# Performance work log

Measured on AMD Instinct MI355X. Metric: run time of the kernel, lower is better.

## Reference

```python
import jax, jax.numpy as jnp
import numpy as np

DIM = 128
HID = 128


def setup_inputs() -> dict:
    key = jax.random.key(0)
    ks = jax.random.split(key, 7)
    x = jax.random.normal(ks[0], (1, 256, 512, DIM), dtype=jnp.float32)
    s = 1.0 / np.sqrt(DIM)
    return {
        "x": x,
        "ln_g": jnp.ones((DIM,), jnp.float32),
        "ln_b": jnp.zeros((DIM,), jnp.float32),
        "w_left": jax.random.normal(ks[1], (DIM, HID), jnp.float32) * s,
        "b_left": jnp.zeros((HID,), jnp.float32),
        "w_right": jax.random.normal(ks[2], (DIM, HID), jnp.float32) * s,
        "b_right": jnp.zeros((HID,), jnp.float32),
        "w_out": jax.random.normal(ks[3], (HID, DIM), jnp.float32) * (1.0 / np.sqrt(HID)),
        "b_out": jnp.zeros((DIM,), jnp.float32),
    }


def reference(x, ln_g, ln_b, w_left, b_left, w_right, b_right, w_out, b_out):
    # LayerNorm over last dim (eps matches torch default 1e-5)
    mu = jnp.mean(x, axis=-1, keepdims=True)
    var = jnp.mean(jnp.square(x - mu), axis=-1, keepdims=True)
    xn = (x - mu) * jax.lax.rsqrt(var + 1e-5) * ln_g + ln_b
    # dual projections: (b, m, i, h)
    left = jnp.einsum('bmid,dh->bmih', xn, w_left) + b_left
    right = jnp.einsum('bmjd,dh->bmjh', xn, w_right) + b_right
    # mean over m of (left_i + right_j) == mean_m(left)_i + mean_m(right)_j
    # (exact algebraic identity; avoids the (b,m,i,j,h) intermediate)
    left_m = jnp.mean(left, axis=1)   # (b, i, h)
    right_m = jnp.mean(right, axis=1)  # (b, j, h)
    outer = left_m[:, :, None, :] + right_m[:, None, :, :]  # (b, i, j, h)
    return jnp.einsum('bijh,hd->bijd', outer, w_out) + b_out
```

## Files before the change

### kernel.cpp

```cpp
#include <hip/hip_runtime.h>
#include <hip/hip_bf16.h>


#define DIM 128
#define NI  512
#define NM  256

__global__ __launch_bounds__(512) void ln_mean_kernel(
    const float* __restrict__ x,
    const float* __restrict__ ln_g,
    const float* __restrict__ ln_b,
    float* __restrict__ S)
{
    const int i    = blockIdx.x;
    const int tid  = threadIdx.x;
    const int lane = tid & 63;
    const int wave = tid >> 6;

    const float g0  = ln_g[2*lane];
    const float g1  = ln_g[2*lane + 1];
    const float be0 = ln_b[2*lane];
    const float be1 = ln_b[2*lane + 1];

    float acc0 = 0.f, acc1 = 0.f;

    #pragma unroll 4
    for (int t = 0; t < NM/8; ++t) {
        const int m = wave + (t << 3);
        const float2 v = *(const float2*)(x + (((size_t)(m * NI + i)) << 7) + 2*lane);

        float s  = v.x + v.y;
        float s2 = v.x*v.x + v.y*v.y;
        #pragma unroll
        for (int off = 32; off; off >>= 1) {
            s  += __shfl_xor(s,  off);
            s2 += __shfl_xor(s2, off);
        }
        const float mu   = s * (1.f/128.f);
        const float var  = s2 * (1.f/128.f) - mu*mu;
        const float rstd = rsqrtf(var + 1e-5f);

        acc0 += (v.x - mu) * rstd * g0 + be0;
        acc1 += (v.y - mu) * rstd * g1 + be1;
    }

    __shared__ float red0[512];
    __shared__ float red1[512];
    red0[tid] = acc0;
    red1[tid] = acc1;
    __syncthreads();

    if (tid < 64) {
        float a0 = 0.f, a1 = 0.f;
        #pragma unroll
        for (int w = 0; w < 8; ++w) {
            a0 += red0[(w << 6) + tid];
            a1 += red1[(w << 6) + tid];
        }
        float2 r;
        r.x = a0 * (1.f/(float)NM);
        r.y = a1 * (1.f/(float)NM);
        *(float2*)(S + ((size_t)i << 7) + 2*tid) = r;
    }
}

__global__ __launch_bounds__(256) void project_kernel(
    const float* __restrict__ S,
    const float* __restrict__ w_left,  const float* __restrict__ b_left,
    const float* __restrict__ w_right, const float* __restrict__ b_right,
    const float* __restrict__ w_out,   const float* __restrict__ b_out,
    float* __restrict__ L, float* __restrict__ R)
{
    const int i   = blockIdx.x;
    const int tid = threadIdx.x;
    const int h   = tid & 127;
    const bool isR = (tid >= 128);

    __shared__ float sS[128];
    __shared__ float sTL[128];
    __shared__ float sTR[128];

    if (tid < 128) sS[tid] = S[((size_t)i << 7) + tid];
    __syncthreads();

    const float* W = isR ? w_right : w_left;
    float acc = isR ? b_right[h] : b_left[h];
    #pragma unroll 8
    for (int d = 0; d < DIM; ++d) {
        acc += sS[d] * W[(d << 7) + h];
    }
    (isR ? sTR : sTL)[h] = acc;
    __syncthreads();

    const float* T = isR ? sTR : sTL;
    float acc2 = isR ? b_out[h] : 0.f;
    #pragma unroll 8
    for (int hh = 0; hh < DIM; ++hh) {
        acc2 += T[hh] * w_out[(hh << 7) + h];
    }
    (isR ? R : L)[((size_t)i << 7) + h] = acc2;
}

__global__ __launch_bounds__(256) void expand_kernel(
    const float4* __restrict__ L4,
    const float4* __restrict__ R4,
    float4* __restrict__ out4)
{
    const size_t t = (size_t)blockIdx.x * 256 + threadIdx.x;
    const int d4 = (int)(t & 31);
    const int j  = (int)((t >> 5) & 511);
    const int i  = (int)(t >> 14);

    const float4 a = L4[(i << 5) + d4];
    const float4 b = R4[(j << 5) + d4];
    float4 o;
    o.x = a.x + b.x;
    o.y = a.y + b.y;
    o.z = a.z + b.z;
    o.w = a.w + b.w;
    out4[t] = o;
}

extern "C" void kernel_launch(void* const* d_in, const int* in_sizes, int n_in,
                              void* d_out, int out_size, void* d_ws, size_t ws_size,
                              hipStream_t stream) {
    const float* x       = (const float*)d_in[0];
    const float* ln_g    = (const float*)d_in[1];
    const float* ln_b    = (const float*)d_in[2];
    const float* w_left  = (const float*)d_in[3];
    const float* b_left  = (const float*)d_in[4];
    const float* w_right = (const float*)d_in[5];
    const float* b_right = (const float*)d_in[6];
    const float* w_out   = (const float*)d_in[7];
    const float* b_out   = (const float*)d_in[8];

    float* S = (float*)d_ws;
    float* L = S + NI * DIM;
    float* R = L + NI * DIM;

    ln_mean_kernel<<<NI, 512, 0, stream>>>(x, ln_g, ln_b, S);
    project_kernel<<<NI, 256, 0, stream>>>(S, w_left, b_left, w_right, b_right,
                                           w_out, b_out, L, R);

    const int total4 = NI * NI * (DIM / 4);
    expand_kernel<<<total4 / 256, 256, 0, stream>>>((const float4*)L,
                                                    (const float4*)R,
                                                    (float4*)d_out);
}
```

Before: 211.3 us.

## Fuse LayerNorm-mean with projections and restructure expand with nontemporal stores

Merges the LayerNorm/mean-over-m kernel and the projection kernel into one launch, dropping the S round-trip and one kernel launch. The LN loop now uses 128-bit vector loads with 32-lane groups instead of 64-lane float2 loads. The expand kernel assigns one block per output row i, loads L once per thread, loops over j, and writes with nontemporal stores to avoid polluting caches on the 128 MB output. In the fused kernel half the threads sit idle during the projection phase.

```diff
diff --git a/kernel.cpp b/kernel.cpp
--- a/kernel.cpp
+++ b/kernel.cpp
@@ -6,119 +6,114 @@
 #define NI  512
 #define NM  256
 
-__global__ __launch_bounds__(512) void ln_mean_kernel(
+typedef float vfloat4 __attribute__((ext_vector_type(4)));
+
+__global__ __launch_bounds__(512) void ln_proj_kernel(
     const float* __restrict__ x,
     const float* __restrict__ ln_g,
     const float* __restrict__ ln_b,
-    float* __restrict__ S)
-{
-    const int i    = blockIdx.x;
-    const int tid  = threadIdx.x;
-    const int lane = tid & 63;
-    const int wave = tid >> 6;
-
-    const float g0  = ln_g[2*lane];
-    const float g1  = ln_g[2*lane + 1];
-    const float be0 = ln_b[2*lane];
-    const float be1 = ln_b[2*lane + 1];
-
-    float acc0 = 0.f, acc1 = 0.f;
-
-    #pragma unroll 4
-    for (int t = 0; t < NM/8; ++t) {
-        const int m = wave + (t << 3);
-        const float2 v = *(const float2*)(x + (((size_t)(m * NI + i)) << 7) + 2*lane);
-
-        float s  = v.x + v.y;
-        float s2 = v.x*v.x + v.y*v.y;
-        #pragma unroll
-        for (int off = 32; off; off >>= 1) {
-            s  += __shfl_xor(s,  off);
-            s2 += __shfl_xor(s2, off);
-        }
-        const float mu   = s * (1.f/128.f);
-        const float var  = s2 * (1.f/128.f) - mu*mu;
-        const float rstd = rsqrtf(var + 1e-5f);
-
-        acc0 += (v.x - mu) * rstd * g0 + be0;
-        acc1 += (v.y - mu) * rstd * g1 + be1;
-    }
-
-    __shared__ float red0[512];
-    __shared__ float red1[512];
-    red0[tid] = acc0;
-    red1[tid] = acc1;
-    __syncthreads();
-
-    if (tid < 64) {
-        float a0 = 0.f, a1 = 0.f;
-        #pragma unroll
-        for (int w = 0; w < 8; ++w) {
-            a0 += red0[(w << 6) + tid];
-            a1 += red1[(w << 6) + tid];
-        }
-        float2 r;
-        r.x = a0 * (1.f/(float)NM);
-        r.y = a1 * (1.f/(float)NM);
-        *(float2*)(S + ((size_t)i << 7) + 2*tid) = r;
-    }
-}
-
-__global__ __launch_bounds__(256) void project_kernel(
-    const float* __restrict__ S,
     const float* __restrict__ w_left,  const float* __restrict__ b_left,
     const float* __restrict__ w_right, const float* __restrict__ b_right,
     const float* __restrict__ w_out,   const float* __restrict__ b_out,
     float* __restrict__ L, float* __restrict__ R)
 {
-    const int i   = blockIdx.x;
-    const int tid = threadIdx.x;
-    const int h   = tid & 127;
-    const bool isR = (tid >= 128);
+    const int i      = blockIdx.x;
+    const int tid    = threadIdx.x;
+    const int lane32 = tid & 31;
+    const int grp    = tid >> 5;
 
-    __shared__ float sS[128];
-    __shared__ float sTL[128];
-    __shared__ float sTR[128];
+    const vfloat4 g4 = *(const vfloat4*)(ln_g + 4 * lane32);
+    const vfloat4 e4 = *(const vfloat4*)(ln_b + 4 * lane32);
 
-    if (tid < 128) sS[tid] = S[((size_t)i << 7) + tid];
+    float a0 = 0.f, a1 = 0.f, a2 = 0.f, a3 = 0.f;
+    const vfloat4* __restrict__ x4 = (const vfloat4*)x;
+
+    #pragma unroll 4
+    for (int t = 0; t < NM / 16; ++t) {
+        const int m = grp + (t << 4);
+        const vfloat4 v = x4[((size_t)(m * NI + i) << 5) + lane32];
+
+        float s  = v.x + v.y + v.z + v.w;
+        float s2 = v.x*v.x + v.y*v.y + v.z*v.z + v.w*v.w;
+        #pragma unroll
+        for (int off = 16; off; off >>= 1) {
+            s  += __shfl_xor(s,  off);
+            s2 += __shfl_xor(s2, off);
+        }
+        const float mu   = s * (1.f/128.f);
+        const float rstd = rsqrtf(s2 * (1.f/128.f) - mu*mu + 1e-5f);
+
+        a0 += (v.x - mu) * rstd * g4.x + e4.x;
+        a1 += (v.y - mu) * rstd * g4.y + e4.y;
+        a2 += (v.z - mu) * rstd * g4.z + e4.z;
+        a3 += (v.w - mu) * rstd * g4.w + e4.w;
+    }
+
+    __shared__ vfloat4 sacc[512];
+    __shared__ float   sS[DIM];
+    __shared__ float   sT[2 * DIM];
+
+    vfloat4 mine;
+    mine.x = a0; mine.y = a1; mine.z = a2; mine.w = a3;
+    sacc[tid] = mine;
     __syncthreads();
 
-    const float* W = isR ? w_right : w_left;
-    float acc = isR ? b_right[h] : b_left[h];
-    #pragma unroll 8
-    for (int d = 0; d < DIM; ++d) {
-        acc += sS[d] * W[(d << 7) + h];
+    if (tid < 32) {
+        vfloat4 t = sacc[tid];
+        #pragma unroll
+        for (int gg = 1; gg < 16; ++gg)
+            t += sacc[(gg << 5) + tid];
+        const float inv = 1.f / (float)NM;
+        sS[4*tid + 0] = t.x * inv;
+        sS[4*tid + 1] = t.y * inv;
+        sS[4*tid + 2] = t.z * inv;
+        sS[4*tid + 3] = t.w * inv;
     }
-    (isR ? sTR : sTL)[h] = acc;
     __syncthreads();
 
-    const float* T = isR ? sTR : sTL;
-    float acc2 = isR ? b_out[h] : 0.f;
-    #pragma unroll 8
-    for (int hh = 0; hh < DIM; ++hh) {
-        acc2 += T[hh] * w_out[(hh << 7) + h];
+    if (tid < 256) {
+        const int  h   = tid & 127;
+        const bool isR = (tid >= 128);
+        const float* __restrict__ W = isR ? w_right : w_left;
+        float acc = isR ? b_right[h] : b_left[h];
+        #pragma unroll 8
+        for (int d = 0; d < DIM; ++d)
+            acc += sS[d] * W[(d << 7) + h];
+        sT[tid] = acc;
     }
-    (isR ? R : L)[((size_t)i << 7) + h] = acc2;
+    __syncthreads();
+
+    if (tid < 256) {
+        const int  h   = tid & 127;
+        const bool isR = (tid >= 128);
+        const float* __restrict__ T = isR ? (sT + DIM) : sT;
+        float acc = isR ? b_out[h] : 0.f;
+        #pragma unroll 8
+        for (int hh = 0; hh < DIM; ++hh)
+            acc += T[hh] * w_out[(hh << 7) + h];
+        (isR ? R : L)[((size_t)i << 7) + h] = acc;
+    }
 }
 
-__global__ __launch_bounds__(256) void expand_kernel(
-    const float4* __restrict__ L4,
-    const float4* __restrict__ R4,
-    float4* __restrict__ out4)
+__global__ __launch_bounds__(512) void expand_kernel(
+    const vfloat4* __restrict__ L4,
+    const vfloat4* __restrict__ R4,
+    vfloat4* __restrict__ out4)
 {
-    const size_t t = (size_t)blockIdx.x * 256 + threadIdx.x;
-    const int d4 = (int)(t & 31);
-    const int j  = (int)((t >> 5) & 511);
-    const int i  = (int)(t >> 14);
+    const int i  = blockIdx.x;
+    const int d4 = threadIdx.x & 31;
+    const int jg = threadIdx.x >> 5;
 
-    const float4 a = L4[(i << 5) + d4];
-    const float4 b = R4[(j << 5) + d4];
-    float4 o;
-    o.x = a.x + b.x;
-    o.y = a.y + b.y;
-    o.z = a.z + b.z;
-    o.w = a.w + b.w;
-    out4[t] = o;
+    const vfloat4 l = L4[(i << 5) + d4];
+    vfloat4* __restrict__ outb = out4 + ((size_t)i << 14);
+
+    #pragma unroll 4
+    for (int it = 0; it < 32; ++it) {
+        const int j = jg + (it << 4);
+        const vfloat4 r = R4[(j << 5) + d4];
+        const vfloat4 o = l + r;
+        __builtin_nontemporal_store(o, &outb[(j << 5) + d4]);
+    }
 }
 
 extern "C" void kernel_launch(void* const* d_in, const int* in_sizes, int n_in,
@@ -134,16 +129,13 @@
     const float* w_out   = (const float*)d_in[7];
     const float* b_out   = (const float*)d_in[8];
 
-    float* S = (float*)d_ws;
-    float* L = S + NI * DIM;
+    float* L = (float*)d_ws;
     float* R = L + NI * DIM;
 
-    ln_mean_kernel<<<NI, 512, 0, stream>>>(x, ln_g, ln_b, S);
-    project_kernel<<<NI, 256, 0, stream>>>(S, w_left, b_left, w_right, b_right,
+    ln_proj_kernel<<<NI, 512, 0, stream>>>(x, ln_g, ln_b,
+                                           w_left, b_left, w_right, b_right,
                                            w_out, b_out, L, R);
-
-    const int total4 = NI * NI * (DIM / 4);
-    expand_kernel<<<total4 / 256, 256, 0, stream>>>((const float4*)L,
-                                                    (const float4*)R,
-                                                    (float4*)d_out);
+    expand_kernel<<<NI, 512, 0, stream>>>((const vfloat4*)L,
+                                          (const vfloat4*)R,
+                                          (vfloat4*)d_out);
 }
```

Result: no change. 213.0 us (+0.8%).
